# Performance work log

Hardware: AMD Instinct MI355X
Metric: run time of the kernel (lower is better)

## Reference

```python
import jax, jax.numpy as jnp
import numpy as np

N, D, H = 32768, 512, 8
HD = D // H  # head_dim = 64
LN_EPS = 1e-5


def setup_inputs() -> dict:
    key = jax.random.key(0)
    ks = jax.random.split(key, 5)
    s = 1.0 / np.sqrt(D)
    return {
        "h": jax.random.normal(ks[0], (N, D), dtype=jnp.float32),
        "Wq": jax.random.normal(ks[1], (D, D), dtype=jnp.float32) * s,
        "Wk": jax.random.normal(ks[2], (D, D), dtype=jnp.float32) * s,
        "Wv": jax.random.normal(ks[3], (D, D), dtype=jnp.float32) * s,
        "Wf": jax.random.normal(ks[4], (D, D), dtype=jnp.float32) * s,
        "ln_gamma": jnp.ones((D,), dtype=jnp.float32),
        "ln_beta": jnp.zeros((D,), dtype=jnp.float32),
    }


def _layernorm(x, g, b):
    mu = jnp.mean(x, axis=-1, keepdims=True)
    var = jnp.mean(jnp.square(x - mu), axis=-1, keepdims=True)
    return (x - mu) * jax.lax.rsqrt(var + LN_EPS) * g + b


def reference(h, Wq, Wk, Wv, Wf, ln_gamma, ln_beta):
    n = h.shape[0]
    # projections (torch Linear y = x @ W^T; weights here stored as [in,out])
    q = jax.nn.relu((h @ Wq).reshape(n, H, HD))
    k = jax.nn.relu((h @ Wk).reshape(n, H, HD))
    v = (h @ Wv).reshape(n, H, HD)
    # per-node outer-product accumulation over heads (n = head axis here)
    kv = jnp.einsum('bnd,bne->bde', k, v)          # [N, HD, HD]
    num = jnp.einsum('bnd,bde->bne', q, kv)        # [N, H, HD]
    denom = jnp.einsum('bnd,bd->bn', q, k.sum(axis=1))  # [N, H]
    attn = num / denom[..., None]                  # [N, H, HD]
    fh = attn.reshape(n, D) @ Wf                   # dropout = identity (eval)
    out = _layernorm(h + fh, ln_gamma, ln_beta)
    return (out, q, k, v)
```

## Files before the change

### kernel.cpp

```cpp
#include <hip/hip_runtime.h>
#include <hip/hip_bf16.h>

#define NROWS 32768
#define DIM   512
#define HEADS 8
#define LN_EPS 1e-5f

typedef __attribute__((ext_vector_type(8))) short short8;
typedef __attribute__((ext_vector_type(4))) float floatx4;

typedef __attribute__((address_space(3))) void lds_void;
typedef __attribute__((address_space(1))) void gbl_void;

__device__ __forceinline__ void async16(const void* g, void* l) {
    __builtin_amdgcn_global_load_lds(
        (gbl_void*)(unsigned long long)(uintptr_t)g,
        (lds_void*)(unsigned int)(uintptr_t)l,
        16, 0, 0);
}

__global__ __launch_bounds__(256) void hconv_kernel(
    const float* __restrict__ h, __hip_bfloat16* __restrict__ hb)
{
    const size_t i = ((size_t)blockIdx.x * 256 + threadIdx.x) * 4;
    const float4 f = *(const float4*)(h + i);
    union { ushort4 u; __hip_bfloat16 b[4]; } pk;
    pk.b[0] = __float2bfloat16(f.x);
    pk.b[1] = __float2bfloat16(f.y);
    pk.b[2] = __float2bfloat16(f.z);
    pk.b[3] = __float2bfloat16(f.w);
    *(ushort4*)(hb + i) = pk.u;
}

__global__ __launch_bounds__(256) void wtrans_kernel(
    const float* __restrict__ Wq, const float* __restrict__ Wk,
    const float* __restrict__ Wv, const float* __restrict__ Wf,
    __hip_bfloat16* __restrict__ Wt)
{
    __shared__ float tile[32][33];
    const int z = blockIdx.z;
    const float* W = (z == 0) ? Wq : (z == 1) ? Wk : (z == 2) ? Wv : Wf;
    __hip_bfloat16* dst = Wt + (size_t)z * DIM * DIM;

    const int bn = blockIdx.x * 32;
    const int bk = blockIdx.y * 32;
    const int tx = threadIdx.x & 31;
    const int ty = threadIdx.x >> 5;
    #pragma unroll
    for (int i = ty; i < 32; i += 8)
        tile[i][tx] = W[(size_t)(bk + i) * DIM + bn + tx];
    __syncthreads();
    #pragma unroll
    for (int i = ty; i < 32; i += 8)
        dst[(size_t)(bn + i) * DIM + bk + tx] = __float2bfloat16(tile[tx][i]);
}

__global__ __launch_bounds__(256) void mfma_gemm_kernel(
    const __hip_bfloat16* __restrict__ A,
    const __hip_bfloat16* __restrict__ Bt,
    float* __restrict__ C, int qkv)
{
    __shared__ __align__(16) char smem[32768];

    const int t    = threadIdx.x;
    const int lane = t & 63;
    const int w    = t >> 6;
    const int wm   = w >> 1, wn = w & 1;
    const int l16  = lane & 15, quad = lane >> 4;
    const int bm   = blockIdx.y * 128;
    const int bx   = blockIdx.x;
    const int bn   = bx * 128;

    float* Cp;
    int ccol, relu;
    if (qkv) {
        Cp   = C + (size_t)(bx >> 2) * ((size_t)NROWS * DIM);
        ccol = (bx & 3) * 128;
        relu = (bx >> 2) < 2;
    } else {
        Cp = C; ccol = bn; relu = 0;
    }

    int offA[4], offB[4];
    char* dA[4]; char* dB[4];
    #pragma unroll
    for (int s = 0; s < 4; ++s) {
        const int p = w * 256 + s * 64 + lane;
        const int r = p >> 3;
        const int c = (p & 7) ^ (r & 7);
        offA[s] = (bm + r) * DIM + c * 8;
        offB[s] = (bn + r) * DIM + c * 8;
        dA[s] = smem + (w * 256 + s * 64) * 16;
        dB[s] = smem + 16384 + (w * 256 + s * 64) * 16;
    }

    int aoff[2][4], boff[2][4];
    #pragma unroll
    for (int kk = 0; kk < 2; ++kk)
        #pragma unroll
        for (int i = 0; i < 4; ++i) {
            const int ra = wm * 64 + i * 16 + l16;
            aoff[kk][i] = (ra * 8 + ((kk * 4 + quad) ^ (ra & 7))) * 16;
            const int rb = wn * 64 + i * 16 + l16;
            boff[kk][i] = 16384 + (rb * 8 + ((kk * 4 + quad) ^ (rb & 7))) * 16;
        }

    floatx4 acc[4][4];
    #pragma unroll
    for (int i = 0; i < 4; ++i)
        #pragma unroll
        for (int j = 0; j < 4; ++j)
            acc[i][j] = (floatx4){0.f, 0.f, 0.f, 0.f};

    for (int k0 = 0; k0 < DIM; k0 += 64) {
        #pragma unroll
        for (int s = 0; s < 4; ++s) async16(A + offA[s] + k0, dA[s]);
        #pragma unroll
        for (int s = 0; s < 4; ++s) async16(Bt + offB[s] + k0, dB[s]);
        __syncthreads();

        #pragma unroll
        for (int kk = 0; kk < 2; ++kk) {
            short8 af[4], bf[4];
            #pragma unroll
            for (int i = 0; i < 4; ++i) af[i] = *(const short8*)(smem + aoff[kk][i]);
            #pragma unroll
            for (int j = 0; j < 4; ++j) bf[j] = *(const short8*)(smem + boff[kk][j]);
            #pragma unroll
            for (int i = 0; i < 4; ++i)
                #pragma unroll
                for (int j = 0; j < 4; ++j)
                    acc[i][j] = __builtin_amdgcn_mfma_f32_16x16x32_bf16(
                        af[i], bf[j], acc[i][j], 0, 0, 0);
        }

        __syncthreads();
    }

    #pragma unroll
    for (int i = 0; i < 4; ++i) {
        const int gr = bm + wm * 64 + i * 16 + quad * 4;
        #pragma unroll
        for (int j = 0; j < 4; ++j) {
            const int gc = ccol + wn * 64 + j * 16 + l16;
            #pragma unroll
            for (int rg = 0; rg < 4; ++rg) {
                float vv = acc[i][j][rg];
                if (relu) vv = fmaxf(vv, 0.f);
                Cp[(size_t)(gr + rg) * DIM + gc] = vv;
            }
        }
    }
}

__global__ __launch_bounds__(256) void attn_kernel(
    const float* __restrict__ q, const float* __restrict__ k,
    const float* __restrict__ v, __hip_bfloat16* __restrict__ attn)
{
    __shared__ float sq[4][8][68];
    __shared__ float sk[4][8][68];
    __shared__ float sv[4][8][68];

    const int t = threadIdx.x;
    const int w = t >> 6, lane = t & 63;
    const size_t base = ((size_t)blockIdx.x * 4 + w) * DIM;

    const int sh = lane >> 3;
    const int sd = (lane & 7) * 8;
    {
        const float4 q0 = ((const float4*)(q + base))[lane * 2];
        const float4 q1 = ((const float4*)(q + base))[lane * 2 + 1];
        const float4 k0 = ((const float4*)(k + base))[lane * 2];
        const float4 k1 = ((const float4*)(k + base))[lane * 2 + 1];
        const float4 v0 = ((const float4*)(v + base))[lane * 2];
        const float4 v1 = ((const float4*)(v + base))[lane * 2 + 1];
        *(float4*)&sq[w][sh][sd]     = q0;
        *(float4*)&sq[w][sh][sd + 4] = q1;
        *(float4*)&sk[w][sh][sd]     = k0;
        *(float4*)&sk[w][sh][sd + 4] = k1;
        *(float4*)&sv[w][sh][sd]     = v0;
        *(float4*)&sv[w][sh][sd + 4] = v1;
    }
    __syncthreads();

    const int n  = lane >> 3;
    const int hh = lane & 7;
    float s = 0.f;
    #pragma unroll
    for (int d = 0; d < 64; d += 4) {
        const float4 a = *(const float4*)&sq[w][n][d];
        const float4 b = *(const float4*)&sk[w][hh][d];
        s += a.x * b.x + a.y * b.y + a.z * b.z + a.w * b.w;
    }
    float den = s;
    den += __shfl_xor(den, 1);
    den += __shfl_xor(den, 2);
    den += __shfl_xor(den, 4);
    const float p = s / den;

    float pl[8];
    #pragma unroll
    for (int h = 0; h < 8; ++h) pl[h] = __shfl(p, (lane & 56) | h);

    const int eg = (lane & 7) * 8;
    float o[8] = {0.f, 0.f, 0.f, 0.f, 0.f, 0.f, 0.f, 0.f};
    #pragma unroll
    for (int h = 0; h < 8; ++h) {
        const float4 v0 = *(const float4*)&sv[w][h][eg];
        const float4 v1 = *(const float4*)&sv[w][h][eg + 4];
        o[0] += pl[h] * v0.x; o[1] += pl[h] * v0.y;
        o[2] += pl[h] * v0.z; o[3] += pl[h] * v0.w;
        o[4] += pl[h] * v1.x; o[5] += pl[h] * v1.y;
        o[6] += pl[h] * v1.z; o[7] += pl[h] * v1.w;
    }
    union { short8 s8; __hip_bfloat16 b[8]; } pk;
    #pragma unroll
    for (int j = 0; j < 8; ++j) pk.b[j] = __float2bfloat16(o[j]);
    *(short8*)(attn + base + (size_t)lane * 8) = pk.s8;
}

__global__ __launch_bounds__(256) void ln_kernel(
    const float* __restrict__ h, const float* fh,
    const float* __restrict__ gamma, const float* __restrict__ beta,
    float* out)
{
    const int lane = threadIdx.x & 63;
    const int wave = threadIdx.x >> 6;
    const size_t base = ((size_t)blockIdx.x * 4 + wave) * DIM;

    const float4 a0 = ((const float4*)(h + base))[lane * 2];
    const float4 a1 = ((const float4*)(h + base))[lane * 2 + 1];
    const float4 b0 = ((const float4*)(fh + base))[lane * 2];
    const float4 b1 = ((const float4*)(fh + base))[lane * 2 + 1];

    float x[8];
    x[0] = a0.x + b0.x; x[1] = a0.y + b0.y; x[2] = a0.z + b0.z; x[3] = a0.w + b0.w;
    x[4] = a1.x + b1.x; x[5] = a1.y + b1.y; x[6] = a1.z + b1.z; x[7] = a1.w + b1.w;

    float s = 0.f;
    #pragma unroll
    for (int i = 0; i < 8; ++i) s += x[i];
    #pragma unroll
    for (int off = 32; off > 0; off >>= 1) s += __shfl_down(s, off);
    const float mu = __shfl(s, 0) * (1.f / DIM);

    float vs = 0.f;
    #pragma unroll
    for (int i = 0; i < 8; ++i) { const float d = x[i] - mu; vs += d * d; }
    #pragma unroll
    for (int off = 32; off > 0; off >>= 1) vs += __shfl_down(vs, off);
    const float rstd = rsqrtf(__shfl(vs, 0) * (1.f / DIM) + LN_EPS);

    const float4 g0 = ((const float4*)gamma)[lane * 2];
    const float4 g1 = ((const float4*)gamma)[lane * 2 + 1];
    const float4 e0 = ((const float4*)beta)[lane * 2];
    const float4 e1 = ((const float4*)beta)[lane * 2 + 1];

    float4 r0, r1;
    r0.x = (x[0] - mu) * rstd * g0.x + e0.x;
    r0.y = (x[1] - mu) * rstd * g0.y + e0.y;
    r0.z = (x[2] - mu) * rstd * g0.z + e0.z;
    r0.w = (x[3] - mu) * rstd * g0.w + e0.w;
    r1.x = (x[4] - mu) * rstd * g1.x + e1.x;
    r1.y = (x[5] - mu) * rstd * g1.y + e1.y;
    r1.z = (x[6] - mu) * rstd * g1.z + e1.z;
    r1.w = (x[7] - mu) * rstd * g1.w + e1.w;

    ((float4*)(out + base))[lane * 2]     = r0;
    ((float4*)(out + base))[lane * 2 + 1] = r1;
}

extern "C" void kernel_launch(void* const* d_in, const int* in_sizes, int n_in,
                              void* d_out, int out_size, void* d_ws, size_t ws_size,
                              hipStream_t stream)
{
    const float* h     = (const float*)d_in[0];
    const float* Wq    = (const float*)d_in[1];
    const float* Wk    = (const float*)d_in[2];
    const float* Wv    = (const float*)d_in[3];
    const float* Wf    = (const float*)d_in[4];
    const float* gamma = (const float*)d_in[5];
    const float* beta  = (const float*)d_in[6];

    const size_t ND = (size_t)NROWS * DIM;
    float* out = (float*)d_out;
    float* qo  = out + ND;
    float* ko  = out + 2 * ND;
    float* vo  = out + 3 * ND;
    float* fh  = out;

    __hip_bfloat16* hb  = (__hip_bfloat16*)d_ws;
    __hip_bfloat16* wt  = hb + ND;
    __hip_bfloat16* wtf = wt + 3 * DIM * DIM;
    __hip_bfloat16* attnb = hb;

    hconv_kernel<<<NROWS * DIM / 1024, 256, 0, stream>>>(h, hb);
    wtrans_kernel<<<dim3(16, 16, 4), 256, 0, stream>>>(Wq, Wk, Wv, Wf, wt);

    mfma_gemm_kernel<<<dim3(12, NROWS / 128), 256, 0, stream>>>(hb, wt, qo, 1);

    attn_kernel<<<NROWS / 4, 256, 0, stream>>>(qo, ko, vo, attnb);

    mfma_gemm_kernel<<<dim3(4, NROWS / 128), 256, 0, stream>>>(attnb, wtf, fh, 0);

    ln_kernel<<<NROWS / 4, 256, 0, stream>>>(h, fh, gamma, beta, out);
}
```

Baseline: 465.5 us.

## Double-buffer GEMM K-tiles with async LDS loads and swizzle block order

Measured after the change: 442.3 us. -5.0%, faster.

```diff
diff --git a/kernel.cpp b/kernel.cpp
--- a/kernel.cpp
+++ b/kernel.cpp
@@ -67,9 +67,15 @@
     const int w    = t >> 6;
     const int wm   = w >> 1, wn = w & 1;
     const int l16  = lane & 15, quad = lane >> 4;
-    const int bm   = blockIdx.y * 128;
-    const int bx   = blockIdx.x;
-    const int bn   = bx * 128;
+
+    const int nwg  = gridDim.x * gridDim.y;
+    int flat = blockIdx.y * gridDim.x + blockIdx.x;
+    flat = (flat & 7) * (nwg >> 3) + (flat >> 3);
+    const int bx = flat % gridDim.x;
+    const int by = flat / gridDim.x;
+
+    const int bm = by * 128;
+    const int bn = bx * 128;
 
     float* Cp;
     int ccol, relu;
@@ -81,29 +87,26 @@
         Cp = C; ccol = bn; relu = 0;
     }
 
-    int offA[4], offB[4];
-    char* dA[4]; char* dB[4];
-    #pragma unroll
-    for (int s = 0; s < 4; ++s) {
-        const int p = w * 256 + s * 64 + lane;
-        const int r = p >> 3;
-        const int c = (p & 7) ^ (r & 7);
-        offA[s] = (bm + r) * DIM + c * 8;
-        offB[s] = (bn + r) * DIM + c * 8;
-        dA[s] = smem + (w * 256 + s * 64) * 16;
-        dB[s] = smem + 16384 + (w * 256 + s * 64) * 16;
-    }
-
-    int aoff[2][4], boff[2][4];
-    #pragma unroll
-    for (int kk = 0; kk < 2; ++kk)
-        #pragma unroll
-        for (int i = 0; i < 4; ++i) {
-            const int ra = wm * 64 + i * 16 + l16;
-            aoff[kk][i] = (ra * 8 + ((kk * 4 + quad) ^ (ra & 7))) * 16;
-            const int rb = wn * 64 + i * 16 + l16;
-            boff[kk][i] = 16384 + (rb * 8 + ((kk * 4 + quad) ^ (rb & 7))) * 16;
-        }
+    const int c0 = w * 128 + lane;
+    const int c1 = c0 + 64;
+    const int r0 = c0 >> 2, kq0 = (c0 & 3) ^ ((r0 >> 1) & 3);
+    const int r1 = c1 >> 2, kq1 = (c1 & 3) ^ ((r1 >> 1) & 3);
+
+    const int offA0 = (bm + r0) * DIM + kq0 * 8;
+    const int offA1 = (bm + r1) * DIM + kq1 * 8;
+    const int offB0 = (bn + r0) * DIM + kq0 * 8;
+    const int offB1 = (bn + r1) * DIM + kq1 * 8;
+    const int ldsC0 = (w * 128) * 16;
+    const int ldsC1 = (w * 128 + 64) * 16;
+
+    int aoff[4], boff[4];
+    #pragma unroll
+    for (int i = 0; i < 4; ++i) {
+        const int ra = wm * 64 + i * 16 + l16;
+        aoff[i] = (ra * 4 + (quad ^ ((ra >> 1) & 3))) * 16;
+        const int rb = wn * 64 + i * 16 + l16;
+        boff[i] = 8192 + (rb * 4 + (quad ^ ((rb >> 1) & 3))) * 16;
+    }
 
     floatx4 acc[4][4];
     #pragma unroll
@@ -112,30 +115,42 @@
         for (int j = 0; j < 4; ++j)
             acc[i][j] = (floatx4){0.f, 0.f, 0.f, 0.f};
 
-    for (int k0 = 0; k0 < DIM; k0 += 64) {
-        #pragma unroll
-        for (int s = 0; s < 4; ++s) async16(A + offA[s] + k0, dA[s]);
-        #pragma unroll
-        for (int s = 0; s < 4; ++s) async16(Bt + offB[s] + k0, dB[s]);
-        __syncthreads();
-
-        #pragma unroll
-        for (int kk = 0; kk < 2; ++kk) {
-            short8 af[4], bf[4];
-            #pragma unroll
-            for (int i = 0; i < 4; ++i) af[i] = *(const short8*)(smem + aoff[kk][i]);
-            #pragma unroll
-            for (int j = 0; j < 4; ++j) bf[j] = *(const short8*)(smem + boff[kk][j]);
-            #pragma unroll
-            for (int i = 0; i < 4; ++i)
-                #pragma unroll
-                for (int j = 0; j < 4; ++j)
-                    acc[i][j] = __builtin_amdgcn_mfma_f32_16x16x32_bf16(
-                        af[i], bf[j], acc[i][j], 0, 0, 0);
-        }
-
-        __syncthreads();
-    }
+    #define STAGE(tt) do {                                                  \
+        char* _b = smem + ((tt) & 1) * 16384;                               \
+        const int _k0 = (tt) * 32;                                          \
+        async16(A  + offA0 + _k0, _b + ldsC0);                              \
+        async16(A  + offA1 + _k0, _b + ldsC1);                              \
+        async16(Bt + offB0 + _k0, _b + 8192 + ldsC0);                       \
+        async16(Bt + offB1 + _k0, _b + 8192 + ldsC1);                       \
+    } while (0)
+
+    #define COMPUTE(tt) do {                                                \
+        const char* _b = smem + ((tt) & 1) * 16384;                         \
+        short8 af[4], bf[4];                                                \
+        _Pragma("unroll")                                                   \
+        for (int i = 0; i < 4; ++i) af[i] = *(const short8*)(_b + aoff[i]); \
+        _Pragma("unroll")                                                   \
+        for (int j = 0; j < 4; ++j) bf[j] = *(const short8*)(_b + boff[j]); \
+        _Pragma("unroll")                                                   \
+        for (int i = 0; i < 4; ++i)                                         \
+            _Pragma("unroll")                                               \
+            for (int j = 0; j < 4; ++j)                                     \
+                acc[i][j] = __builtin_amdgcn_mfma_f32_16x16x32_bf16(        \
+                    af[i], bf[j], acc[i][j], 0, 0, 0);                      \
+    } while (0)
+
+    STAGE(0);
+    for (int kt = 0; kt < 15; ++kt) {
+        STAGE(kt + 1);
+        asm volatile("s_waitcnt vmcnt(4)\n\ts_barrier" ::: "memory");
+        COMPUTE(kt);
+        asm volatile("s_barrier" ::: "memory");
+    }
+    asm volatile("s_waitcnt vmcnt(0)\n\ts_barrier" ::: "memory");
+    COMPUTE(15);
+
+    #undef STAGE
+    #undef COMPUTE
 
     #pragma unroll
     for (int i = 0; i < 4; ++i) {
```
